# Kernel optimization log

Hardware: AMD Instinct MI355X
Metric: run time of the kernel (lower is better)

Reference implementation:

```python
import jax, jax.numpy as jnp
import numpy as np

DEPTH, HEADS, DIM_HEAD = 6, 8, 64
B, N, E = 2, 128, 160
NUM_ATOMS, NF = 100, 127
DIM = NF + 1                 # 128, node feature dim fed to transformer
INNER = HEADS * DIM_HEAD     # 512


def setup_inputs() -> dict:
    key = jax.random.key(0)
    ks = iter(jax.random.split(key, 40))
    f32 = jnp.float32
    def w(shape, scale=0.02):
        return jax.random.normal(next(ks), shape, dtype=f32) * scale
    inp = {
        "indices": jax.random.randint(next(ks), (B, N), 0, NUM_ATOMS),
        "coordinates": jax.random.normal(next(ks), (B, N, 3), dtype=f32),
        "bonds": jax.random.randint(next(ks), (E, 2), 0, N),
        "noise_level": jax.random.uniform(next(ks), (1,), dtype=f32),
        "atom_emb": w((NUM_ATOMS, NF), 1.0),
        "ln1_g": jnp.ones((DEPTH, DIM), f32), "ln1_b": jnp.zeros((DEPTH, DIM), f32),
        "Wq": w((DEPTH, DIM, INNER)), "bq": jnp.zeros((DEPTH, INNER), f32),
        "Wkv": w((DEPTH, DIM, 2 * INNER)), "bkv": jnp.zeros((DEPTH, 2 * INNER), f32),
        "We": w((DEPTH, 3, INNER)), "be": jnp.zeros((DEPTH, INNER), f32),
        "Wo": w((DEPTH, INNER, DIM)), "bo": jnp.zeros((DEPTH, DIM), f32),
        "Wg1": w((DEPTH, 3 * DIM, 1)),
        "ln2_g": jnp.ones((DEPTH, DIM), f32), "ln2_b": jnp.zeros((DEPTH, DIM), f32),
        "W1": w((DEPTH, DIM, 4 * DIM)), "b1": jnp.zeros((DEPTH, 4 * DIM), f32),
        "W2": w((DEPTH, 4 * DIM, DIM)), "b2": jnp.zeros((DEPTH, DIM), f32),
        "Wg2": w((DEPTH, 3 * DIM, 1)),
        "Wlin": w((DIM, 1)), "blin": jnp.zeros((1,), f32),
    }
    return inp


def _ln(x, g, b, eps=1e-5):
    m = jnp.mean(x, -1, keepdims=True)
    v = jnp.mean((x - m) ** 2, -1, keepdims=True)
    return (x - m) * jax.lax.rsqrt(v + eps) * g + b


def _gated_residual(x, res, Wg):
    # gate = sigmoid(Linear([x, res, x-res])); out = x*gate + res*(1-gate)
    gate = jax.nn.sigmoid(jnp.concatenate([x, res, x - res], -1) @ Wg)  # (B,N,1)
    return x * gate + res * (1.0 - gate)


def _forward(indices, bonds, coordinates, noise_level, atom_emb,
             ln1_g, ln1_b, Wq, bq, Wkv, bkv, We, be, Wo, bo, Wg1,
             ln2_g, ln2_b, W1, b1, W2, b2, Wg2, Wlin, blin):
    b, n = indices.shape
    # nodes_embedding: atom embedding + noise-level channel
    noise = jnp.broadcast_to(noise_level.reshape(1, 1, 1).astype(coordinates.dtype), (b, n, 1))
    nodes = jnp.concatenate([atom_emb[indices], noise], -1)  # (B,N,DIM)
    # edges_embedding: vectorized scatter of per-bond coordinate differences
    i, j = bonds[:, 0], bonds[:, 1]
    diff = coordinates[:, i] - coordinates[:, j]             # (B,E,3)
    edges = jnp.zeros((b, n, n, 3), coordinates.dtype)
    edges = edges.at[:, i, j].set(diff).at[:, j, i].set(-diff)

    scale = DIM_HEAD ** -0.5
    for l in range(DEPTH):
        # PreNorm + edge-biased attention (mask is all-ones -> no-op)
        xn = _ln(nodes, ln1_g[l], ln1_b[l])
        q = (xn @ Wq[l] + bq[l]).reshape(b, n, HEADS, DIM_HEAD)
        k, v = jnp.split(xn @ Wkv[l] + bkv[l], 2, -1)
        k = k.reshape(b, n, HEADS, DIM_HEAD)
        v = v.reshape(b, n, HEADS, DIM_HEAD)
        e = (edges @ We[l] + be[l]).reshape(b, n, n, HEADS, DIM_HEAD)
        kk = k[:, None] + e                                   # (B,i,j,H,D)
        vv = v[:, None] + e
        sim = jnp.einsum('bihd,bijhd->bijh', q, kk) * scale
        attn = jax.nn.softmax(sim, axis=2)                    # softmax over j
        out = jnp.einsum('bijh,bijhd->bihd', attn, vv).reshape(b, n, INNER)
        out = out @ Wo[l] + bo[l]
        nodes = _gated_residual(out, nodes, Wg1[l])
        # PreNorm + FeedForward (exact GELU, mult=4) + gated residual
        xn = _ln(nodes, ln2_g[l], ln2_b[l])
        ff = jax.nn.gelu(xn @ W1[l] + b1[l], approximate=False) @ W2[l] + b2[l]
        nodes = _gated_residual(ff, nodes, Wg2[l])
    return jnp.sum(nodes @ Wlin + blin)


def reference(indices, coordinates, bonds, noise_level, atom_emb,
              ln1_g, ln1_b, Wq, bq, Wkv, bkv, We, be, Wo, bo, Wg1,
              ln2_g, ln2_b, W1, b1, W2, b2, Wg2, Wlin, blin):
    return _forward(indices, bonds, coordinates, noise_level, atom_emb,
                    ln1_g, ln1_b, Wq, bq, Wkv, bkv, We, be, Wo, bo, Wg1,
                    ln2_g, ln2_b, W1, b1, W2, b2, Wg2, Wlin, blin)
```

## Files before the change

### kernel.cpp

```cpp
#include <hip/hip_runtime.h>
#include <hip/hip_fp16.h>
#include <math.h>

#define DEPTH 6
#define HEADS 8
#define BB    2
#define NN    128
#define EE    160
#define NF    127
#define DIMM  128
#define INNER 512
#define NNODE 256

__device__ __forceinline__ void gload16(const void* g, void* l) {
    __builtin_amdgcn_global_load_lds((const __attribute__((address_space(1))) void*)g,
                                     (__attribute__((address_space(3))) void*)l,
                                     16, 0, 0);
}

__device__ __forceinline__ void wait_vm0() { __builtin_amdgcn_s_waitcnt(0x0f70); }

__device__ __forceinline__ void wstage16(const char* gslice, char* ldsslice, int ln) {
#pragma unroll
    for (int i = 0; i < 16; i++)
        gload16(gslice + i * 1024 + ln * 16, ldsslice + i * 1024);
}
__device__ __forceinline__ void wstage16s(const char* gslice, int rowstride,
                                          char* ldsslice, int ln) {
#pragma unroll
    for (int i = 0; i < 16; i++)
        gload16(gslice + (size_t)i * rowstride + ln * 16, ldsslice + i * 1024);
}

__device__ __forceinline__ void fma8h(float4& a0, float4& a1, float s, float4 raw) {
    const __half2* hp = (const __half2*)&raw;
    float2 p0 = __half22float2(hp[0]), p1 = __half22float2(hp[1]);
    float2 p2 = __half22float2(hp[2]), p3 = __half22float2(hp[3]);
    a0.x += s * p0.x; a0.y += s * p0.y; a0.z += s * p1.x; a0.w += s * p1.y;
    a1.x += s * p2.x; a1.y += s * p2.y; a1.z += s * p3.x; a1.w += s * p3.y;
}

__device__ __forceinline__ void gemv512(const float* act, const float* wbuf,
                                        float* s_part, int w, int ln) {
    float4 a0 = {0,0,0,0}, a1 = {0,0,0,0};
    const float4* w4 = (const float4*)wbuf;
#pragma unroll
    for (int r = 0; r < 16; r++)
        fma8h(a0, a1, act[w * 16 + r], w4[r * 64 + ln]);
    ((float4*)(s_part + w * 512))[ln * 2]     = a0;
    ((float4*)(s_part + w * 512))[ln * 2 + 1] = a1;
}

__device__ __forceinline__ void gemv128(const float* act, const float* wbuf,
                                        float* s_part, int w, int ln) {
    float2 acc = {0, 0};
#pragma unroll 8
    for (int r = 0; r < 64; r++) {
        float raw = wbuf[r * 64 + ln];
        __half2 h = *(__half2*)&raw;
        float2 p = __half22float2(h);
        float a = act[w * 64 + r];
        acc.x += a * p.x; acc.y += a * p.y;
    }
    s_part[w * 128 + ln * 2]     = acc.x;
    s_part[w * 128 + ln * 2 + 1] = acc.y;
}

__device__ __forceinline__ float block_reduce_sum_8w(float val, float* sbuf) {
#pragma unroll
    for (int off = 32; off > 0; off >>= 1) val += __shfl_xor(val, off, 64);
    int wave = threadIdx.x >> 6;
    if ((threadIdx.x & 63) == 0) sbuf[wave] = val;
    __syncthreads();
    float r = sbuf[0] + sbuf[1] + sbuf[2] + sbuf[3] + sbuf[4] + sbuf[5] + sbuf[6] + sbuf[7];
    __syncthreads();
    return r;
}

__device__ void qkv_wave(int t, int bn, int layer,
                         const __half* hWq, const float* bq,
                         const __half* hWkv, const float* bkv,
                         float* qb, __half* hk, __half* hv,
                         const float* s_xn, float* s_part, float* arena) {
    int w = t >> 6, ln = t & 63;
    char*  lslice = (char*)arena + w * 16384;
    float* wbuf   = arena + w * 4096;

    const char* WqL = (const char*)(hWq + (size_t)layer * DIMM * INNER);
    wstage16(WqL + w * 16384, lslice, ln);
    wait_vm0();
    gemv512(s_xn, wbuf, s_part, w, ln);
    __syncthreads();
    {
        float q = bq[layer * INNER + t];
#pragma unroll
        for (int g = 0; g < 8; g++) q += s_part[g * 512 + t];
        qb[(size_t)bn * INNER + t] = q;
    }
    __syncthreads();

    const char* WkvL = (const char*)(hWkv + (size_t)layer * DIMM * 2 * INNER);
    wstage16s(WkvL + (size_t)(w * 16) * 2048, 2048, lslice, ln);
    wait_vm0();
    gemv512(s_xn, wbuf, s_part, w, ln);
    __syncthreads();
    {
        float k = bkv[layer * 2 * INNER + t];
#pragma unroll
        for (int g = 0; g < 8; g++) k += s_part[g * 512 + t];
        hk[(size_t)bn * INNER + t] = __float2half(k);
    }
    __syncthreads();

    wstage16s(WkvL + (size_t)(w * 16) * 2048 + 1024, 2048, lslice, ln);
    wait_vm0();
    gemv512(s_xn, wbuf, s_part, w, ln);
    __syncthreads();
    {
        float v = bkv[layer * 2 * INNER + INNER + t];
#pragma unroll
        for (int g = 0; g < 8; g++) v += s_part[g * 512 + t];
        hv[(size_t)bn * INNER + t] = __float2half(v);
    }
    __syncthreads();
}


__global__ __launch_bounds__(512) void k_cvt(const float* Wq, const float* Wkv,
                                             const float* Wo, const float* W1,
                                             const float* W2,
                                             __half* hWq, __half* hWkv, __half* hWo,
                                             __half* hW1, __half* hW2) {
    int g = blockIdx.x * 512 + threadIdx.x;
    const float4* src; __half* dst; int off;
    if (g < 98304)       { src = (const float4*)Wq;  dst = hWq;  off = g; }
    else if (g < 294912) { src = (const float4*)Wkv; dst = hWkv; off = g - 98304; }
    else if (g < 393216) { src = (const float4*)Wo;  dst = hWo;  off = g - 294912; }
    else if (g < 491520) { src = (const float4*)W1;  dst = hW1;  off = g - 393216; }
    else                 { src = (const float4*)W2;  dst = hW2;  off = g - 491520; }
    float4 v = src[off];
    __half2* d2 = (__half2*)(dst + (size_t)off * 4);
    d2[0] = __floats2half2_rn(v.x, v.y);
    d2[1] = __floats2half2_rn(v.z, v.w);
}

__global__ __launch_bounds__(512, 1) void k_pre(const int* indices, const float* noise,
                                                const float* atom_emb,
                                                const float* ln1_g, const float* ln1_b,
                                                const __half* hWq, const float* bq,
                                                const __half* hWkv, const float* bkv,
                                                float* nodes, float* qb,
                                                __half* hk, __half* hv) {
    int bn = blockIdx.x;
    int t  = threadIdx.x;
    int d  = t & 127;
    bool own = (t < 128);
    __shared__ float arena[32768];
    __shared__ float s_xn[128];
    __shared__ float s_red[8];
    __shared__ float s_part[4096];

    float nd = 0.0f;
    if (own) {
        int idx = indices[bn];
        nd = (d < NF) ? atom_emb[idx * NF + d] : noise[0];
        nodes[bn * DIMM + d] = nd;
    }
    float m   = block_reduce_sum_8w(own ? nd : 0.0f, s_red) * (1.0f / 128.0f);
    float df  = nd - m;
    float var = block_reduce_sum_8w(own ? df * df : 0.0f, s_red) * (1.0f / 128.0f);
    if (own) s_xn[d] = df * rsqrtf(var + 1e-5f) * ln1_g[d] + ln1_b[d];
    __syncthreads();

    qkv_wave(t, bn, 0, hWq, bq, hWkv, bkv, qb, hk, hv, s_xn, s_part, arena);
}

__global__ __launch_bounds__(512, 1) void k_layer(int l,
        const float* coords, const int* bonds,
        const float* We, const float* be,
        float* qb, const __half* hkin, const __half* hvin,
        __half* hkout, __half* hvout,
        const __half* hWo, const float* bo, const float* Wg1,
        const float* ln2_g, const float* ln2_b,
        const __half* hW1, const float* b1,
        const __half* hW2, const float* b2,
        const float* Wg2,
        const float* ln1_g, const float* ln1_b,
        const __half* hWq, const float* bq,
        const __half* hWkv, const float* bkv,
        float* nodes) {
    int bn = blockIdx.x;
    int b = bn >> 7, i = bn & 127;
    int t = threadIdx.x;
    int d = t & 127;
    bool own = (t < 128);
    int w = t >> 6, ln = t & 63;

    __shared__ float arena[32768];
    __shared__ float scoord[384];
    __shared__ float sedge[384];
    __shared__ int   sadj[128];
    __shared__ float s_l[32];
    __shared__ float s_ao[512];
    __shared__ float s_h[512];
    __shared__ float s_xn[128];
    __shared__ float s_red[8];
    __shared__ float s_part[4096];
    float* s_o = arena;
    char*  lslice = (char*)arena + w * 16384;
    float* wbuf   = arena + w * 4096;

    int jg = t >> 7, c = t & 127, h = c >> 4;
    const float4* qR  = (const float4*)(qb + (size_t)bn * INNER);
    const float4* WeR = (const float4*)(We + (size_t)l * 3 * INNER);
    float4 qv  = qR[c];
    float4 we0 = WeR[c], we1 = WeR[128 + c], we2 = WeR[256 + c];
    float4 bev = ((const float4*)(be + (size_t)l * INNER))[c];
    float res = own ? nodes[bn * DIMM + d] : 0.0f;

    if (t < 3 * NN) scoord[t] = coords[b * 3 * NN + t];
    if (t < NN) sadj[t] = 0;
    __syncthreads();
    if (t < EE) {
        int e0 = bonds[2 * t], e1 = bonds[2 * t + 1];
        if (e0 == i) sadj[e1] = 1;
        if (e1 == i) sadj[e0] = 1;
    }
    __syncthreads();
    if (t < NN) {
        int j = t;
        float msk = sadj[j] ? 1.0f : 0.0f;
        sedge[3 * j + 0] = msk * (scoord[3 * i + 0] - scoord[3 * j + 0]);
        sedge[3 * j + 1] = msk * (scoord[3 * i + 1] - scoord[3 * j + 1]);
        sedge[3 * j + 2] = msk * (scoord[3 * i + 2] - scoord[3 * j + 2]);
    }
    __syncthreads();

    const float2* kR2 = (const float2*)(hkin + (size_t)b * NN * INNER);
    const float2* vR2 = (const float2*)(hvin + (size_t)b * NN * INNER);
    float l_run = 0.0f;
    float4 o_run = {0, 0, 0, 0};
    int j0 = jg * 32;
#pragma unroll
    for (int base = 0; base < 32; base += 8) {
        float2 kraw[8], vraw[8];
#pragma unroll
        for (int p = 0; p < 8; p++) {
            int j = j0 + base + p;
            kraw[p] = kR2[j * 128 + c];
            vraw[p] = vR2[j * 128 + c];
        }
#pragma unroll
        for (int p = 0; p < 8; p++) {
            int j = j0 + base + p;
            float ex = sedge[3 * j], ey = sedge[3 * j + 1], ez = sedge[3 * j + 2];
            float4 e;
            e.x = bev.x + ex * we0.x + ey * we1.x + ez * we2.x;
            e.y = bev.y + ex * we0.y + ey * we1.y + ez * we2.y;
            e.z = bev.z + ex * we0.z + ey * we1.z + ez * we2.z;
            e.w = bev.w + ex * we0.w + ey * we1.w + ez * we2.w;
            const __half2* kh = (const __half2*)&kraw[p];
            float2 k01 = __half22float2(kh[0]), k23 = __half22float2(kh[1]);
            float s = (qv.x * (k01.x + e.x) + qv.y * (k01.y + e.y))
                    + (qv.z * (k23.x + e.z) + qv.w * (k23.y + e.w));
            s += __shfl_xor(s, 1, 64);
            s += __shfl_xor(s, 2, 64);
            s += __shfl_xor(s, 4, 64);
            s += __shfl_xor(s, 8, 64);
            float pp = __expf(s * 0.125f);
            const __half2* vh = (const __half2*)&vraw[p];
            float2 v01 = __half22float2(vh[0]), v23 = __half22float2(vh[1]);
            l_run += pp;
            o_run.x += pp * (v01.x + e.x);
            o_run.y += pp * (v01.y + e.y);
            o_run.z += pp * (v23.x + e.z);
            o_run.w += pp * (v23.y + e.w);
        }
    }
    ((float4*)(s_o + jg * INNER))[c] = o_run;
    if ((c & 15) == 0) s_l[jg * HEADS + h] = l_run;
    __syncthreads();
    if (jg == 0) {
        float4 o = o_run;
        float lsum = l_run;
#pragma unroll
        for (int g = 1; g < 4; g++) {
            float4 og = ((float4*)(s_o + g * INNER))[c];
            o.x += og.x; o.y += og.y; o.z += og.z; o.w += og.w;
            lsum += s_l[g * HEADS + h];
        }
        float inv = 1.0f / lsum;
        float4 rr; rr.x = o.x * inv; rr.y = o.y * inv; rr.z = o.z * inv; rr.w = o.w * inv;
        ((float4*)s_ao)[c] = rr;
    }
    __syncthreads();

    const char* WoL = (const char*)(hWo + (size_t)l * INNER * DIMM);
    wstage16(WoL + w * 16384, lslice, ln);
    wait_vm0();
    gemv128(s_ao, wbuf, s_part, w, ln);
    __syncthreads();
    float x = 0.0f;
    if (own) {
        x = bo[l * DIMM + d];
#pragma unroll
        for (int g = 0; g < 8; g++) x += s_part[g * 128 + d];
    }
    __syncthreads();

    const float* Wg1_l = Wg1 + l * 3 * DIMM;
    float texpr = own ? (x * Wg1_l[d] + res * Wg1_l[DIMM + d] + (x - res) * Wg1_l[2 * DIMM + d]) : 0.0f;
    float g1 = block_reduce_sum_8w(texpr, s_red);
    g1 = 1.0f / (1.0f + __expf(-g1));
    float n1 = x * g1 + res * (1.0f - g1);

    float m   = block_reduce_sum_8w(own ? n1 : 0.0f, s_red) * (1.0f / 128.0f);
    float df  = n1 - m;
    float var = block_reduce_sum_8w(own ? df * df : 0.0f, s_red) * (1.0f / 128.0f);
    if (own) s_xn[d] = df * rsqrtf(var + 1e-5f) * ln2_g[l * DIMM + d] + ln2_b[l * DIMM + d];
    __syncthreads();

    const char* W1L = (const char*)(hW1 + (size_t)l * DIMM * 4 * DIMM);
    wstage16(W1L + w * 16384, lslice, ln);
    wait_vm0();
    gemv512(s_xn, wbuf, s_part, w, ln);
    __syncthreads();
    {
        float a = b1[l * 4 * DIMM + t];
#pragma unroll
        for (int g = 0; g < 8; g++) a += s_part[g * 512 + t];
        a = 0.5f * a * (1.0f + erff(a * 0.70710678f));
        s_h[t] = a;
    }
    __syncthreads();

    const char* W2L = (const char*)(hW2 + (size_t)l * 4 * DIMM * DIMM);
    wstage16(W2L + w * 16384, lslice, ln);
    wait_vm0();
    gemv128(s_h, wbuf, s_part, w, ln);
    __syncthreads();
    float y = 0.0f;
    if (own) {
        y = b2[l * DIMM + d];
#pragma unroll
        for (int g = 0; g < 8; g++) y += s_part[g * 128 + d];
    }
    __syncthreads();

    const float* Wg2_l = Wg2 + l * 3 * DIMM;
    texpr = own ? (y * Wg2_l[d] + n1 * Wg2_l[DIMM + d] + (y - n1) * Wg2_l[2 * DIMM + d]) : 0.0f;
    float g2 = block_reduce_sum_8w(texpr, s_red);
    g2 = 1.0f / (1.0f + __expf(-g2));
    float n2 = y * g2 + n1 * (1.0f - g2);
    if (own) nodes[bn * DIMM + d] = n2;

    if (l < DEPTH - 1) {
        float m1   = block_reduce_sum_8w(own ? n2 : 0.0f, s_red) * (1.0f / 128.0f);
        float df1  = n2 - m1;
        float var1 = block_reduce_sum_8w(own ? df1 * df1 : 0.0f, s_red) * (1.0f / 128.0f);
        if (own) s_xn[d] = df1 * rsqrtf(var1 + 1e-5f) * ln1_g[(l + 1) * DIMM + d]
                         + ln1_b[(l + 1) * DIMM + d];
        __syncthreads();
        qkv_wave(t, bn, l + 1, hWq, bq, hWkv, bkv, qb, hkout, hvout,
                 s_xn, s_part, arena);
    }
}

__global__ __launch_bounds__(256) void k_final(const float* nodes, const float* Wlin,
                                               const float* blin, float* out) {
    int t = threadIdx.x;
    __shared__ float s_w[DIMM];
    if (t < DIMM) s_w[t] = Wlin[t];
    __syncthreads();
    float s = blin[0];
    const float4* nr = (const float4*)(nodes + t * DIMM);
#pragma unroll 8
    for (int q = 0; q < 32; q++) {
        float4 n = nr[q];
        s += n.x * s_w[4 * q] + n.y * s_w[4 * q + 1] + n.z * s_w[4 * q + 2] + n.w * s_w[4 * q + 3];
    }
#pragma unroll
    for (int off = 32; off > 0; off >>= 1) s += __shfl_xor(s, off, 64);
    __shared__ float sb[4];
    int wave = t >> 6, lane = t & 63;
    if (lane == 0) sb[wave] = s;
    __syncthreads();
    if (t == 0) out[0] = sb[0] + sb[1] + sb[2] + sb[3];
}

extern "C" void kernel_launch(void* const* d_in, const int* in_sizes, int n_in,
                              void* d_out, int out_size, void* d_ws, size_t ws_size,
                              hipStream_t stream) {
    const int*   indices = (const int*)d_in[0];
    const float* coords  = (const float*)d_in[1];
    const int*   bonds   = (const int*)d_in[2];
    const float* noise   = (const float*)d_in[3];
    const float* atom_emb= (const float*)d_in[4];
    const float* ln1_g   = (const float*)d_in[5];
    const float* ln1_b   = (const float*)d_in[6];
    const float* Wq      = (const float*)d_in[7];
    const float* bq      = (const float*)d_in[8];
    const float* Wkv     = (const float*)d_in[9];
    const float* bkv     = (const float*)d_in[10];
    const float* We      = (const float*)d_in[11];
    const float* be      = (const float*)d_in[12];
    const float* Wo      = (const float*)d_in[13];
    const float* bo      = (const float*)d_in[14];
    const float* Wg1     = (const float*)d_in[15];
    const float* ln2_g   = (const float*)d_in[16];
    const float* ln2_b   = (const float*)d_in[17];
    const float* W1      = (const float*)d_in[18];
    const float* b1      = (const float*)d_in[19];
    const float* W2      = (const float*)d_in[20];
    const float* b2      = (const float*)d_in[21];
    const float* Wg2     = (const float*)d_in[22];
    const float* Wlin    = (const float*)d_in[23];
    const float* blin    = (const float*)d_in[24];

    float*  ws    = (float*)d_ws;
    float*  nodes = ws;
    float*  qb    = nodes + NNODE * DIMM;
    __half* hkb   = (__half*)(qb + NNODE * INNER);
    __half* hvb   = hkb + 2 * NNODE * INNER;
    __half* hWq   = hvb + 2 * NNODE * INNER;
    __half* hWkv  = hWq + DEPTH * DIMM * INNER;
    __half* hWo   = hWkv + DEPTH * DIMM * 2 * INNER;
    __half* hW1   = hWo + DEPTH * INNER * DIMM;
    __half* hW2   = hW1 + DEPTH * DIMM * 4 * DIMM;

    k_cvt<<<1152, 512, 0, stream>>>(Wq, Wkv, Wo, W1, W2, hWq, hWkv, hWo, hW1, hW2);
    k_pre<<<NNODE, 512, 0, stream>>>(indices, noise, atom_emb, ln1_g, ln1_b,
                                     hWq, bq, hWkv, bkv, nodes, qb, hkb, hvb);
    for (int l = 0; l < DEPTH; l++) {
        const __half* hkin = hkb + (size_t)(l & 1) * NNODE * INNER;
        const __half* hvin = hvb + (size_t)(l & 1) * NNODE * INNER;
        __half* hkout = hkb + (size_t)((l + 1) & 1) * NNODE * INNER;
        __half* hvout = hvb + (size_t)((l + 1) & 1) * NNODE * INNER;
        k_layer<<<NNODE, 512, 0, stream>>>(l, coords, bonds, We, be,
                                           qb, hkin, hvin, hkout, hvout,
                                           hWo, bo, Wg1, ln2_g, ln2_b, hW1, b1, hW2, b2,
                                           Wg2, ln1_g, ln1_b, hWq, bq, hWkv, bkv, nodes);
    }
    k_final<<<1, 256, 0, stream>>>(nodes, Wlin, blin, (float*)d_out);
}
```

Baseline: 286.0 us.

## Prefetch next GEMV weight slice into LDS while current GEMV computes

Weight staging through global_load_lds is reordered so that each weight matrix (Wo, W1, W2, next-layer Wq, Wkv halves) is issued right after the previous GEMV finishes reading LDS, instead of just before its own use. The Wo load now starts at kernel entry, overlapping the attention phase, and s_o moves from arena to s_part so the prefetched slice isn't overwritten. The aim is to hide global memory latency behind attention, reductions and layernorm work. It depends on careful waitcnt placement (lgkm wait before overwriting the LDS slice) and on s_part not being reused while the attention partials live there.

```diff
diff --git a/kernel.cpp b/kernel.cpp
--- a/kernel.cpp
+++ b/kernel.cpp
@@ -19,6 +19,7 @@
 }
 
 __device__ __forceinline__ void wait_vm0() { __builtin_amdgcn_s_waitcnt(0x0f70); }
+__device__ __forceinline__ void wait_lgkm0() { __builtin_amdgcn_s_waitcnt(0xC07F); }
 
 __device__ __forceinline__ void wstage16(const char* gslice, char* ldsslice, int ln) {
 #pragma unroll
@@ -75,54 +76,6 @@
     float r = sbuf[0] + sbuf[1] + sbuf[2] + sbuf[3] + sbuf[4] + sbuf[5] + sbuf[6] + sbuf[7];
     __syncthreads();
     return r;
-}
-
-__device__ void qkv_wave(int t, int bn, int layer,
-                         const __half* hWq, const float* bq,
-                         const __half* hWkv, const float* bkv,
-                         float* qb, __half* hk, __half* hv,
-                         const float* s_xn, float* s_part, float* arena) {
-    int w = t >> 6, ln = t & 63;
-    char*  lslice = (char*)arena + w * 16384;
-    float* wbuf   = arena + w * 4096;
-
-    const char* WqL = (const char*)(hWq + (size_t)layer * DIMM * INNER);
-    wstage16(WqL + w * 16384, lslice, ln);
-    wait_vm0();
-    gemv512(s_xn, wbuf, s_part, w, ln);
-    __syncthreads();
-    {
-        float q = bq[layer * INNER + t];
-#pragma unroll
-        for (int g = 0; g < 8; g++) q += s_part[g * 512 + t];
-        qb[(size_t)bn * INNER + t] = q;
-    }
-    __syncthreads();
-
-    const char* WkvL = (const char*)(hWkv + (size_t)layer * DIMM * 2 * INNER);
-    wstage16s(WkvL + (size_t)(w * 16) * 2048, 2048, lslice, ln);
-    wait_vm0();
-    gemv512(s_xn, wbuf, s_part, w, ln);
-    __syncthreads();
-    {
-        float k = bkv[layer * 2 * INNER + t];
-#pragma unroll
-        for (int g = 0; g < 8; g++) k += s_part[g * 512 + t];
-        hk[(size_t)bn * INNER + t] = __float2half(k);
-    }
-    __syncthreads();
-
-    wstage16s(WkvL + (size_t)(w * 16) * 2048 + 1024, 2048, lslice, ln);
-    wait_vm0();
-    gemv512(s_xn, wbuf, s_part, w, ln);
-    __syncthreads();
-    {
-        float v = bkv[layer * 2 * INNER + INNER + t];
-#pragma unroll
-        for (int g = 0; g < 8; g++) v += s_part[g * 512 + t];
-        hv[(size_t)bn * INNER + t] = __float2half(v);
-    }
-    __syncthreads();
 }
 
 
@@ -155,10 +108,17 @@
     int t  = threadIdx.x;
     int d  = t & 127;
     bool own = (t < 128);
+    int w = t >> 6, ln = t & 63;
     __shared__ float arena[32768];
     __shared__ float s_xn[128];
     __shared__ float s_red[8];
     __shared__ float s_part[4096];
+    char*  lslice = (char*)arena + w * 16384;
+    float* wbuf   = arena + w * 4096;
+
+    const char* WqL  = (const char*)(hWq + 0);
+    const char* WkvL = (const char*)(hWkv + 0);
+    wstage16(WqL + w * 16384, lslice, ln);
 
     float nd = 0.0f;
     if (own) {
@@ -172,7 +132,41 @@
     if (own) s_xn[d] = df * rsqrtf(var + 1e-5f) * ln1_g[d] + ln1_b[d];
     __syncthreads();
 
-    qkv_wave(t, bn, 0, hWq, bq, hWkv, bkv, qb, hk, hv, s_xn, s_part, arena);
+    wait_vm0();
+    gemv512(s_xn, wbuf, s_part, w, ln);
+    wait_lgkm0();
+    wstage16s(WkvL + (size_t)(w * 16) * 2048, 2048, lslice, ln);
+    __syncthreads();
+    {
+        float q = bq[t];
+#pragma unroll
+        for (int g = 0; g < 8; g++) q += s_part[g * 512 + t];
+        qb[(size_t)bn * INNER + t] = q;
+    }
+    __syncthreads();
+
+    wait_vm0();
+    gemv512(s_xn, wbuf, s_part, w, ln);
+    wait_lgkm0();
+    wstage16s(WkvL + (size_t)(w * 16) * 2048 + 1024, 2048, lslice, ln);
+    __syncthreads();
+    {
+        float k = bkv[t];
+#pragma unroll
+        for (int g = 0; g < 8; g++) k += s_part[g * 512 + t];
+        hk[(size_t)bn * INNER + t] = __float2half(k);
+    }
+    __syncthreads();
+
+    wait_vm0();
+    gemv512(s_xn, wbuf, s_part, w, ln);
+    __syncthreads();
+    {
+        float v = bkv[INNER + t];
+#pragma unroll
+        for (int g = 0; g < 8; g++) v += s_part[g * 512 + t];
+        hv[(size_t)bn * INNER + t] = __float2half(v);
+    }
 }
 
 __global__ __launch_bounds__(512, 1) void k_layer(int l,
@@ -206,9 +200,17 @@
     __shared__ float s_xn[128];
     __shared__ float s_red[8];
     __shared__ float s_part[4096];
-    float* s_o = arena;
+    float* s_o = s_part;
     char*  lslice = (char*)arena + w * 16384;
     float* wbuf   = arena + w * 4096;
+
+    const char* WoL  = (const char*)(hWo + (size_t)l * INNER * DIMM);
+    const char* W1L  = (const char*)(hW1 + (size_t)l * DIMM * 4 * DIMM);
+    const char* W2L  = (const char*)(hW2 + (size_t)l * 4 * DIMM * DIMM);
+    const char* WqL  = (const char*)(hWq + (size_t)(l + 1) * DIMM * INNER);
+    const char* WkvL = (const char*)(hWkv + (size_t)(l + 1) * DIMM * 2 * INNER);
+
+    wstage16(WoL + w * 16384, lslice, ln);
 
     int jg = t >> 7, c = t & 127, h = c >> 4;
     const float4* qR  = (const float4*)(qb + (size_t)bn * INNER);
@@ -295,10 +297,10 @@
     }
     __syncthreads();
 
-    const char* WoL = (const char*)(hWo + (size_t)l * INNER * DIMM);
-    wstage16(WoL + w * 16384, lslice, ln);
     wait_vm0();
     gemv128(s_ao, wbuf, s_part, w, ln);
+    wait_lgkm0();
+    wstage16(W1L + w * 16384, lslice, ln);
     __syncthreads();
     float x = 0.0f;
     if (own) {
@@ -320,10 +322,10 @@
     if (own) s_xn[d] = df * rsqrtf(var + 1e-5f) * ln2_g[l * DIMM + d] + ln2_b[l * DIMM + d];
     __syncthreads();
 
-    const char* W1L = (const char*)(hW1 + (size_t)l * DIMM * 4 * DIMM);
-    wstage16(W1L + w * 16384, lslice, ln);
     wait_vm0();
     gemv512(s_xn, wbuf, s_part, w, ln);
+    wait_lgkm0();
+    wstage16(W2L + w * 16384, lslice, ln);
     __syncthreads();
     {
         float a = b1[l * 4 * DIMM + t];
@@ -334,10 +336,10 @@
     }
     __syncthreads();
 
-    const char* W2L = (const char*)(hW2 + (size_t)l * 4 * DIMM * DIMM);
-    wstage16(W2L + w * 16384, lslice, ln);
     wait_vm0();
     gemv128(s_h, wbuf, s_part, w, ln);
+    wait_lgkm0();
+    if (l < DEPTH - 1) wstage16(WqL + w * 16384, lslice, ln);
     __syncthreads();
     float y = 0.0f;
     if (own) {
@@ -361,8 +363,42 @@
         if (own) s_xn[d] = df1 * rsqrtf(var1 + 1e-5f) * ln1_g[(l + 1) * DIMM + d]
                          + ln1_b[(l + 1) * DIMM + d];
         __syncthreads();
-        qkv_wave(t, bn, l + 1, hWq, bq, hWkv, bkv, qb, hkout, hvout,
-                 s_xn, s_part, arena);
+
+        wait_vm0();
+        gemv512(s_xn, wbuf, s_part, w, ln);
+        wait_lgkm0();
+        wstage16s(WkvL + (size_t)(w * 16) * 2048, 2048, lslice, ln);
+        __syncthreads();
+        {
+            float q = bq[(l + 1) * INNER + t];
+#pragma unroll
+            for (int g = 0; g < 8; g++) q += s_part[g * 512 + t];
+            qb[(size_t)bn * INNER + t] = q;
+        }
+        __syncthreads();
+
+        wait_vm0();
+        gemv512(s_xn, wbuf, s_part, w, ln);
+        wait_lgkm0();
+        wstage16s(WkvL + (size_t)(w * 16) * 2048 + 1024, 2048, lslice, ln);
+        __syncthreads();
+        {
+            float k = bkv[(l + 1) * 2 * INNER + t];
+#pragma unroll
+            for (int g = 0; g < 8; g++) k += s_part[g * 512 + t];
+            hkout[(size_t)bn * INNER + t] = __float2half(k);
+        }
+        __syncthreads();
+
+        wait_vm0();
+        gemv512(s_xn, wbuf, s_part, w, ln);
+        __syncthreads();
+        {
+            float v = bkv[(l + 1) * 2 * INNER + INNER + t];
+#pragma unroll
+            for (int g = 0; g < 8; g++) v += s_part[g * 512 + t];
+            hvout[(size_t)bn * INNER + t] = __float2half(v);
+        }
     }
 }
 
```

New measurement: 281.9 us. About the same (-1.5%).
